# Kernel tuning notes

Hardware: AMD Instinct MI355X
Metric: run time of the kernel (lower is better)

Reference implementation:

```python
import jax, jax.numpy as jnp
import numpy as np

E, D, H, F = 3, 512, 8, 2048
B, V, L = 32, 21, 128
DH = D // H
EPS = 1e-5


def setup_inputs() -> dict:
    key = jax.random.key(0)
    ks = jax.random.split(key, 8)
    s = 0.02
    def p(k, shape):
        return (jax.random.normal(k, shape, jnp.float32) * s)
    return {
        "x": jax.random.normal(ks[0], (B, V, L, D), jnp.float32),
        "Wq": p(ks[1], (E, D, D)), "bq": jnp.zeros((E, D), jnp.float32),
        "Wk": p(ks[2], (E, D, D)), "bk": jnp.zeros((E, D), jnp.float32),
        "Wv": p(ks[3], (E, D, D)), "bv": jnp.zeros((E, D), jnp.float32),
        "Wo": p(ks[4], (E, D, D)), "bo": jnp.zeros((E, D), jnp.float32),
        "W1": p(ks[5], (E, D, F)), "b1": jnp.zeros((E, F), jnp.float32),
        "W2": p(ks[6], (E, F, D)), "b2": jnp.zeros((E, D), jnp.float32),
        "g1": jnp.ones((E, D), jnp.float32), "be1": jnp.zeros((E, D), jnp.float32),
        "g2": jnp.ones((E, D), jnp.float32), "be2": jnp.zeros((E, D), jnp.float32),
    }


def _batchnorm(x, gamma, beta):
    # x: [N, L, D]; BatchNorm1d(d_model) on x.transpose(-2,-1) == per-D-channel
    # stats over (N, L) axes (train-mode, biased variance).
    mean = jnp.mean(x, axis=(0, 1))
    var = jnp.var(x, axis=(0, 1))
    return (x - mean) * jax.lax.rsqrt(var + EPS) * gamma + beta


def _layer(x, prev_scores, Wq, bq, Wk, bk, Wv, bv, Wo, bo,
           W1, b1, W2, b2, g1, be1, g2, be2):
    N = x.shape[0]
    # multi-head projections -> [N, H, L, DH]
    q = (x @ Wq + bq).reshape(N, L, H, DH).transpose(0, 2, 1, 3)
    k = (x @ Wk + bk).reshape(N, L, H, DH).transpose(0, 2, 1, 3)
    v = (x @ Wv + bv).reshape(N, L, H, DH).transpose(0, 2, 1, 3)
    scores = jnp.einsum('nhld,nhmd->nhlm', q, k) / jnp.sqrt(jnp.float32(DH))
    if prev_scores is not None:
        scores = scores + prev_scores  # RealFormer-style residual score add
    attn = jax.nn.softmax(scores, axis=-1)
    ctx = jnp.einsum('nhlm,nhmd->nhld', attn, v)
    ctx = ctx.transpose(0, 2, 1, 3).reshape(N, L, D)
    x_ = ctx @ Wo + bo
    x = _batchnorm(x + x_, g1, be1)
    ffn = jax.nn.gelu(x @ W1 + b1, approximate=False) @ W2 + b2
    x = _batchnorm(x + ffn, g2, be2)
    return x, scores


def reference(x, Wq, bq, Wk, bk, Wv, bv, Wo, bo, W1, b1, W2, b2,
              g1, be1, g2, be2):
    h = x.reshape(-1, L, D)  # (B*V, L, D)
    scores = None
    for i in range(E):
        h, scores = _layer(h, scores,
                           Wq[i], bq[i], Wk[i], bk[i], Wv[i], bv[i],
                           Wo[i], bo[i], W1[i], b1[i], W2[i], b2[i],
                           g1[i], be1[i], g2[i], be2[i])
    return h
```

## Files before the change

### kernel.cpp

```cpp
#include <hip/hip_runtime.h>
#include <hip/hip_bf16.h>


typedef unsigned short u16;
typedef unsigned int u32;
typedef __attribute__((ext_vector_type(8))) short short8;
typedef __attribute__((ext_vector_type(4))) float floatx4;

#define DEV static __device__ __forceinline__

DEV u16 f2bf(float f) {
    union { float f; u32 u; } a; a.f = f;
    u32 r = a.u + 0x7FFF + ((a.u >> 16) & 1);
    return (u16)(r >> 16);
}
DEV float bf2f(u16 b) {
    union { u32 u; float f; } a; a.u = ((u32)b) << 16; return a.f;
}

DEV void gload16(const void* g, void* l) {
    __builtin_amdgcn_global_load_lds((const __attribute__((address_space(1))) void*)g,
                                     (__attribute__((address_space(3))) void*)l, 16, 0, 0);
}

__global__ void wtrans(const float* __restrict__ W, u16* __restrict__ out, int K, int N) {
    __shared__ float tile[32][33];
    const int k0 = blockIdx.x * 32, n0 = blockIdx.y * 32;
    const int tx = threadIdx.x & 31, ty = threadIdx.x >> 5;
#pragma unroll
    for (int j = 0; j < 4; ++j) {
        int r = ty + j * 8;
        tile[r][tx] = W[(size_t)(k0 + r) * N + n0 + tx];
    }
    __syncthreads();
#pragma unroll
    for (int j = 0; j < 4; ++j) {
        int r = ty + j * 8;
        out[(size_t)(n0 + r) * K + k0 + tx] = f2bf(tile[tx][r]);
    }
}

__global__ void bias_concat(const float* __restrict__ bq, const float* __restrict__ bk,
                            const float* __restrict__ bv, float* __restrict__ bqkv) {
    int t = blockIdx.x * 256 + threadIdx.x;
    if (t >= 3 * 1536) return;
    int e = t / 1536, c = t % 1536;
    float v = (c < 512) ? bq[e * 512 + c] : (c < 1024) ? bk[e * 512 + c - 512] : bv[e * 512 + c - 1024];
    bqkv[t] = v;
}

__global__ void xconvert(const float* __restrict__ x, u16* __restrict__ hb) {
    size_t i = ((size_t)blockIdx.x * 256 + threadIdx.x) * 8;
    float4 v0 = *(const float4*)&x[i];
    float4 v1 = *(const float4*)&x[i + 4];
    short8 o;
    o[0] = (short)f2bf(v0.x); o[1] = (short)f2bf(v0.y); o[2] = (short)f2bf(v0.z); o[3] = (short)f2bf(v0.w);
    o[4] = (short)f2bf(v1.x); o[5] = (short)f2bf(v1.y); o[6] = (short)f2bf(v1.z); o[7] = (short)f2bf(v1.w);
    *(short8*)&hb[i] = o;
}

template <int EPI>
__global__ __launch_bounds__(512)
void gemm_bt(const u16* __restrict__ A, int lda, const u16* __restrict__ Bt,
             const float* __restrict__ bias, const u16* __restrict__ res,
             u16* __restrict__ out, int N, int K) {
    __shared__ u16 sA[128 * 32];
    __shared__ u16 sB[128 * 32];
    const int tid = threadIdx.x;
    const int wave = tid >> 6, lane = tid & 63;
    const int wm = wave >> 2, wn = wave & 3;
    const int m0 = blockIdx.y * 128, n0 = blockIdx.x * 128;
    const int fr = lane & 15, fq = lane >> 4;
    const int srow = lane >> 2, scol = (lane & 3) * 8;

    floatx4 acc[4][2] = {};

    for (int k0 = 0; k0 < K; k0 += 32) {
        __syncthreads();
        {
            int ra = wave * 16 + srow;
            gload16(A + (size_t)(m0 + ra) * lda + k0 + scol, &sA[wave * 512]);
            gload16(Bt + (size_t)(n0 + ra) * K + k0 + scol, &sB[wave * 512]);
        }
        __syncthreads();
        short8 af[4], bfr[2];
#pragma unroll
        for (int m = 0; m < 4; ++m)
            af[m] = *(const short8*)&sA[(wm * 64 + m * 16 + fr) * 32 + fq * 8];
#pragma unroll
        for (int nn = 0; nn < 2; ++nn)
            bfr[nn] = *(const short8*)&sB[(wn * 32 + nn * 16 + fr) * 32 + fq * 8];
#pragma unroll
        for (int m = 0; m < 4; ++m)
#pragma unroll
            for (int nn = 0; nn < 2; ++nn)
                acc[m][nn] = __builtin_amdgcn_mfma_f32_16x16x32_bf16(af[m], bfr[nn], acc[m][nn], 0, 0, 0);
    }

#pragma unroll
    for (int nn = 0; nn < 2; ++nn) {
        int col = n0 + wn * 32 + nn * 16 + fr;
        float bv = bias[col];
#pragma unroll
        for (int m = 0; m < 4; ++m) {
            int rowb = m0 + wm * 64 + m * 16 + fq * 4;
#pragma unroll
            for (int r = 0; r < 4; ++r) {
                size_t idx = (size_t)(rowb + r) * N + col;
                float v = acc[m][nn][r] + bv;
                if (EPI == 2) {
                    v += bf2f(res[idx]);
                } else if (EPI == 1) {
                    v = 0.5f * v * (1.f + erff(v * 0.70710678118f));
                }
                out[idx] = f2bf(v);
            }
        }
    }
}

template <int HAS_PREV, int STORE_S>
__global__ __launch_bounds__(256)
void attn_kernel(u16* __restrict__ qkv, u16* __restrict__ scores) {
    const int bid = blockIdx.x;
    const int n = bid >> 3, h = bid & 7;
    const int tid = threadIdx.x, wave = tid >> 6, lane = tid & 63;
    const int wm = wave >> 1, wn = wave & 1;
    const int fr = lane & 15, fq = lane >> 4;

    __shared__ __align__(16) u16 uni[128 * 136];
    __shared__ __align__(16) u16 sV[64 * 136];
    __shared__ float sRed[128 * 2];

    u16 (*sQK)[128 * 32] = (u16(*)[128 * 32])uni;

    {
        const int t_ = wave;
        const int qk = t_ >> 1, kh = t_ & 1;
        const u16* base = qkv + (size_t)n * 128 * 1536 + qk * 512 + h * 64 + kh * 32 + (lane & 3) * 8;
        u16* dst = &sQK[t_][0];
        const int rr = lane >> 2;
#pragma unroll
        for (int c = 0; c < 8; ++c)
            gload16(base + (size_t)(c * 16 + rr) * 1536, dst + c * 512);
    }
    for (int i = 0; i < 32; ++i) {
        int idx = i * 256 + tid;
        int dh = idx & 63, m = idx >> 6;
        sV[dh * 136 + m] = qkv[(size_t)(n * 128 + m) * 1536 + 1024 + h * 64 + dh];
    }
    __syncthreads();

    floatx4 acc[4][4] = {};
#pragma unroll
    for (int kh = 0; kh < 2; ++kh) {
        short8 a[4], b[4];
#pragma unroll
        for (int m = 0; m < 4; ++m)
            a[m] = *(const short8*)&sQK[kh][(wm * 64 + m * 16 + fr) * 32 + fq * 8];
#pragma unroll
        for (int nn = 0; nn < 4; ++nn)
            b[nn] = *(const short8*)&sQK[2 + kh][(wn * 64 + nn * 16 + fr) * 32 + fq * 8];
#pragma unroll
        for (int m = 0; m < 4; ++m)
#pragma unroll
            for (int nn = 0; nn < 4; ++nn)
                acc[m][nn] = __builtin_amdgcn_mfma_f32_16x16x32_bf16(a[m], b[nn], acc[m][nn], 0, 0, 0);
    }

    const size_t sbase = (size_t)bid * 128 * 128;
#pragma unroll
    for (int m = 0; m < 4; ++m)
#pragma unroll
        for (int r = 0; r < 4; ++r) {
            int row = wm * 64 + m * 16 + fq * 4 + r;
#pragma unroll
            for (int nn = 0; nn < 4; ++nn) {
                int col = wn * 64 + nn * 16 + fr;
                float v = acc[m][nn][r] * 0.125f;
                if (HAS_PREV) v += bf2f(scores[sbase + (size_t)row * 128 + col]);
                if (STORE_S) scores[sbase + (size_t)row * 128 + col] = f2bf(v);
                acc[m][nn][r] = v;
            }
        }

#pragma unroll
    for (int m = 0; m < 4; ++m)
#pragma unroll
        for (int r = 0; r < 4; ++r) {
            float mx = fmaxf(fmaxf(acc[m][0][r], acc[m][1][r]), fmaxf(acc[m][2][r], acc[m][3][r]));
#pragma unroll
            for (int d = 1; d < 16; d <<= 1) mx = fmaxf(mx, __shfl_xor(mx, d));
            if (fr == 0) sRed[(wm * 64 + m * 16 + fq * 4 + r) * 2 + wn] = mx;
        }
    __syncthreads();

    float rmax[4][4];
#pragma unroll
    for (int m = 0; m < 4; ++m)
#pragma unroll
        for (int r = 0; r < 4; ++r) {
            int row = wm * 64 + m * 16 + fq * 4 + r;
            rmax[m][r] = fmaxf(sRed[row * 2], sRed[row * 2 + 1]);
        }
    __syncthreads();

    u16* sP = uni;
#pragma unroll
    for (int m = 0; m < 4; ++m)
#pragma unroll
        for (int r = 0; r < 4; ++r) {
            int row = wm * 64 + m * 16 + fq * 4 + r;
            float sm = 0.f;
#pragma unroll
            for (int nn = 0; nn < 4; ++nn) {
                float p = __expf(acc[m][nn][r] - rmax[m][r]);
                acc[m][nn][r] = p;
                sm += p;
            }
#pragma unroll
            for (int d = 1; d < 16; d <<= 1) sm += __shfl_xor(sm, d);
            if (fr == 0) sRed[row * 2 + wn] = sm;
#pragma unroll
            for (int nn = 0; nn < 4; ++nn)
                sP[row * 136 + wn * 64 + nn * 16 + fr] = f2bf(acc[m][nn][r]);
        }
    __syncthreads();

    floatx4 acc2[4][2] = {};
#pragma unroll
    for (int k0 = 0; k0 < 128; k0 += 32) {
        short8 a[4], b[2];
#pragma unroll
        for (int m = 0; m < 4; ++m)
            a[m] = *(const short8*)&sP[(wm * 64 + m * 16 + fr) * 136 + k0 + fq * 8];
#pragma unroll
        for (int n2 = 0; n2 < 2; ++n2)
            b[n2] = *(const short8*)&sV[(wn * 32 + n2 * 16 + fr) * 136 + k0 + fq * 8];
#pragma unroll
        for (int m = 0; m < 4; ++m)
#pragma unroll
            for (int n2 = 0; n2 < 2; ++n2)
                acc2[m][n2] = __builtin_amdgcn_mfma_f32_16x16x32_bf16(a[m], b[n2], acc2[m][n2], 0, 0, 0);
    }

#pragma unroll
    for (int m = 0; m < 4; ++m)
#pragma unroll
        for (int r = 0; r < 4; ++r) {
            int row = wm * 64 + m * 16 + fq * 4 + r;
            float inv = 1.f / (sRed[row * 2] + sRed[row * 2 + 1]);
#pragma unroll
            for (int n2 = 0; n2 < 2; ++n2) {
                int col = wn * 32 + n2 * 16 + fr;
                qkv[(size_t)(n * 128 + row) * 1536 + h * 64 + col] = f2bf(acc2[m][n2][r] * inv);
            }
        }
}

__global__ void zero_stats(float* s) { s[threadIdx.x] = 0.f; }

__global__ void bn_stats(const u16* __restrict__ y, float* __restrict__ stats, int M) {
    const int t = threadIdx.x;
    const int c0 = t * 2;
    float s0 = 0, s1 = 0, q0 = 0, q1 = 0;
    for (int r = blockIdx.x; r < M; r += gridDim.x) {
        u32 v = *(const u32*)&y[(size_t)r * 512 + c0];
        float a = bf2f((u16)(v & 0xffff)), b = bf2f((u16)(v >> 16));
        s0 += a; s1 += b; q0 += a * a; q1 += b * b;
    }
    atomicAdd(&stats[c0], s0);
    atomicAdd(&stats[c0 + 1], s1);
    atomicAdd(&stats[512 + c0], q0);
    atomicAdd(&stats[512 + c0 + 1], q1);
}

__global__ void bn_finalize(float* stats, int M) {
    int c = blockIdx.x * 256 + threadIdx.x;
    if (c >= 512) return;
    float mean = stats[c] / M;
    float var = stats[512 + c] / M - mean * mean;
    stats[c] = mean;
    stats[512 + c] = rsqrtf(var + 1e-5f);
}

template <int FINAL>
__global__ void bn_apply(const u16* __restrict__ y, const float* __restrict__ stats,
                         const float* __restrict__ gamma, const float* __restrict__ beta,
                         u16* __restrict__ outb, float* __restrict__ outf) {
    size_t i = ((size_t)blockIdx.x * 256 + threadIdx.x) * 8;
    short8 v = *(const short8*)&y[i];
    int c = (int)(i & 511);
    float o[8];
#pragma unroll
    for (int j = 0; j < 8; ++j) {
        float f = bf2f((u16)v[j]);
        o[j] = (f - stats[c + j]) * stats[512 + c + j] * gamma[c + j] + beta[c + j];
    }
    if (FINAL) {
        float4 a = { o[0], o[1], o[2], o[3] }, b = { o[4], o[5], o[6], o[7] };
        *(float4*)&outf[i] = a;
        *(float4*)&outf[i + 4] = b;
    } else {
        short8 ob;
#pragma unroll
        for (int j = 0; j < 8; ++j) ob[j] = (short)f2bf(o[j]);
        *(short8*)&outb[i] = ob;
    }
}

extern "C" void kernel_launch(void* const* d_in, const int* in_sizes, int n_in,
                              void* d_out, int out_size, void* d_ws, size_t ws_size,
                              hipStream_t stream) {
    const float* x  = (const float*)d_in[0];
    const float* Wq = (const float*)d_in[1];  const float* bq = (const float*)d_in[2];
    const float* Wk = (const float*)d_in[3];  const float* bk = (const float*)d_in[4];
    const float* Wv = (const float*)d_in[5];  const float* bv = (const float*)d_in[6];
    const float* Wo = (const float*)d_in[7];  const float* bo = (const float*)d_in[8];
    const float* W1 = (const float*)d_in[9];  const float* b1 = (const float*)d_in[10];
    const float* W2 = (const float*)d_in[11]; const float* b2 = (const float*)d_in[12];
    const float* g1 = (const float*)d_in[13]; const float* be1 = (const float*)d_in[14];
    const float* g2 = (const float*)d_in[15]; const float* be2 = (const float*)d_in[16];

    const int M = 86016;
    const int MC = 43008;

    char* ws = (char*)d_ws;
    size_t off = 0;
    auto alloc = [&](size_t bytes) -> void* {
        void* p = ws + off;
        off = (off + bytes + 255) & ~(size_t)255;
        return p;
    };
    u16* scores = (u16*)alloc((size_t)5376 * 16384 * 2);
    u16* hb     = (u16*)alloc((size_t)M * 512 * 2);
    u16* qkv    = (u16*)alloc((size_t)M * 1536 * 2);
    u16* Wqkvt  = (u16*)alloc((size_t)3 * 1536 * 512 * 2);
    u16* Wot    = (u16*)alloc((size_t)3 * 512 * 512 * 2);
    u16* W1t    = (u16*)alloc((size_t)3 * 2048 * 512 * 2);
    u16* W2t    = (u16*)alloc((size_t)3 * 512 * 2048 * 2);
    float* bqkv = (float*)alloc((size_t)3 * 1536 * 4);
    float* stats = (float*)alloc(1024 * 4);

    if (off > ws_size) return;

    for (int e = 0; e < 3; ++e) {
        wtrans<<<dim3(16, 16), 256, 0, stream>>>(Wq + (size_t)e * 512 * 512, Wqkvt + (size_t)e * 1536 * 512, 512, 512);
        wtrans<<<dim3(16, 16), 256, 0, stream>>>(Wk + (size_t)e * 512 * 512, Wqkvt + (size_t)e * 1536 * 512 + 512 * 512, 512, 512);
        wtrans<<<dim3(16, 16), 256, 0, stream>>>(Wv + (size_t)e * 512 * 512, Wqkvt + (size_t)e * 1536 * 512 + 1024 * 512, 512, 512);
        wtrans<<<dim3(16, 16), 256, 0, stream>>>(Wo + (size_t)e * 512 * 512, Wot + (size_t)e * 512 * 512, 512, 512);
        wtrans<<<dim3(16, 64), 256, 0, stream>>>(W1 + (size_t)e * 512 * 2048, W1t + (size_t)e * 2048 * 512, 512, 2048);
        wtrans<<<dim3(64, 16), 256, 0, stream>>>(W2 + (size_t)e * 2048 * 512, W2t + (size_t)e * 512 * 2048, 2048, 512);
    }
    bias_concat<<<18, 256, 0, stream>>>(bq, bk, bv, bqkv);
    xconvert<<<21504, 256, 0, stream>>>(x, hb);

    for (int e = 0; e < 3; ++e) {
        gemm_bt<0><<<dim3(12, 672), 512, 0, stream>>>(hb, 512, Wqkvt + (size_t)e * 1536 * 512,
                                                      bqkv + e * 1536, nullptr, qkv, 1536, 512);
        if (e == 0)      attn_kernel<0, 1><<<5376, 256, 0, stream>>>(qkv, scores);
        else if (e == 1) attn_kernel<1, 1><<<5376, 256, 0, stream>>>(qkv, scores);
        else             attn_kernel<1, 0><<<5376, 256, 0, stream>>>(qkv, scores);
        gemm_bt<2><<<dim3(4, 672), 512, 0, stream>>>(qkv, 1536, Wot + (size_t)e * 512 * 512,
                                                     bo + e * 512, hb, hb, 512, 512);
        zero_stats<<<1, 1024, 0, stream>>>(stats);
        bn_stats<<<512, 256, 0, stream>>>(hb, stats, M);
        bn_finalize<<<2, 256, 0, stream>>>(stats, M);
        bn_apply<0><<<21504, 256, 0, stream>>>(hb, stats, g1 + e * 512, be1 + e * 512, hb, nullptr);
        for (int c = 0; c < 2; ++c) {
            const u16* hc = hb + (size_t)c * MC * 512;
            gemm_bt<1><<<dim3(16, 336), 512, 0, stream>>>(hc, 512, W1t + (size_t)e * 2048 * 512,
                                                          b1 + e * 2048, nullptr, qkv, 2048, 512);
            gemm_bt<2><<<dim3(4, 336), 512, 0, stream>>>(qkv, 2048, W2t + (size_t)e * 512 * 2048,
                                                         b2 + e * 512, hc, (u16*)hc, 512, 2048);
        }
        zero_stats<<<1, 1024, 0, stream>>>(stats);
        bn_stats<<<512, 256, 0, stream>>>(hb, stats, M);
        bn_finalize<<<2, 256, 0, stream>>>(stats, M);
        if (e < 2)
            bn_apply<0><<<21504, 256, 0, stream>>>(hb, stats, g2 + e * 512, be2 + e * 512, hb, nullptr);
        else
            bn_apply<1><<<21504, 256, 0, stream>>>(hb, stats, g2 + e * 512, be2 + e * 512, nullptr, (float*)d_out);
    }
    (void)in_sizes; (void)n_in; (void)out_size;
}
```

Before: 3.983 ms.

## Fuse BatchNorm statistics into GEMM epilogue and vectorize attention score/V loads

BatchNorm sum and sum-of-squares are now accumulated in the residual GEMM epilogue, reduced across lanes by shuffles and added with atomics, so the separate bn_stats pass over the activations is gone. The attention kernel now loads V with 16-byte vector reads before transposing into shared memory. It also stores the residual scores in a per-thread fragment-ordered layout so they can be read and written as contiguous short8 vectors. The trade-offs are more global atomics from every GEMM tile and statistics computed from unrounded float values rather than the stored bf16.

```diff
diff --git a/kernel.cpp b/kernel.cpp
--- a/kernel.cpp
+++ b/kernel.cpp
@@ -63,7 +63,7 @@
 __global__ __launch_bounds__(512)
 void gemm_bt(const u16* __restrict__ A, int lda, const u16* __restrict__ Bt,
              const float* __restrict__ bias, const u16* __restrict__ res,
-             u16* __restrict__ out, int N, int K) {
+             u16* __restrict__ out, int N, int K, float* __restrict__ stats) {
     __shared__ u16 sA[128 * 32];
     __shared__ u16 sB[128 * 32];
     const int tid = threadIdx.x;
@@ -97,6 +97,7 @@
                 acc[m][nn] = __builtin_amdgcn_mfma_f32_16x16x32_bf16(af[m], bfr[nn], acc[m][nn], 0, 0, 0);
     }
 
+    float ssum[2] = { 0.f, 0.f }, sqsum[2] = { 0.f, 0.f };
 #pragma unroll
     for (int nn = 0; nn < 2; ++nn) {
         int col = n0 + wn * 32 + nn * 16 + fr;
@@ -110,10 +111,25 @@
                 float v = acc[m][nn][r] + bv;
                 if (EPI == 2) {
                     v += bf2f(res[idx]);
+                    ssum[nn] += v;
+                    sqsum[nn] += v * v;
                 } else if (EPI == 1) {
                     v = 0.5f * v * (1.f + erff(v * 0.70710678118f));
                 }
                 out[idx] = f2bf(v);
+            }
+        }
+    }
+    if (EPI == 2) {
+#pragma unroll
+        for (int nn = 0; nn < 2; ++nn) {
+            float s = ssum[nn], q = sqsum[nn];
+            s += __shfl_xor(s, 16); s += __shfl_xor(s, 32);
+            q += __shfl_xor(q, 16); q += __shfl_xor(q, 32);
+            if (fq == 0) {
+                int col = n0 + wn * 32 + nn * 16 + fr;
+                atomicAdd(&stats[col], s);
+                atomicAdd(&stats[512 + col], q);
             }
         }
     }
@@ -144,10 +160,17 @@
         for (int c = 0; c < 8; ++c)
             gload16(base + (size_t)(c * 16 + rr) * 1536, dst + c * 512);
     }
-    for (int i = 0; i < 32; ++i) {
-        int idx = i * 256 + tid;
-        int dh = idx & 63, m = idx >> 6;
-        sV[dh * 136 + m] = qkv[(size_t)(n * 128 + m) * 1536 + 1024 + h * 64 + dh];
+    {
+        const int mrow = tid >> 1;
+        const int dh0 = (tid & 1) * 32;
+        const u16* vsrc = qkv + (size_t)(n * 128 + mrow) * 1536 + 1024 + h * 64 + dh0;
+#pragma unroll
+        for (int j = 0; j < 4; ++j) {
+            short8 vv = *(const short8*)&vsrc[j * 8];
+#pragma unroll
+            for (int e2 = 0; e2 < 8; ++e2)
+                sV[(dh0 + j * 8 + e2) * 136 + mrow] = (u16)vv[e2];
+        }
     }
     __syncthreads();
 
@@ -168,21 +191,37 @@
                 acc[m][nn] = __builtin_amdgcn_mfma_f32_16x16x32_bf16(a[m], b[nn], acc[m][nn], 0, 0, 0);
     }
 
-    const size_t sbase = (size_t)bid * 128 * 128;
-#pragma unroll
-    for (int m = 0; m < 4; ++m)
-#pragma unroll
-        for (int r = 0; r < 4; ++r) {
-            int row = wm * 64 + m * 16 + fq * 4 + r;
-#pragma unroll
-            for (int nn = 0; nn < 4; ++nn) {
-                int col = wn * 64 + nn * 16 + fr;
+    const size_t tbase = ((size_t)bid * 256 + tid) * 64;
+#pragma unroll
+    for (int m = 0; m < 4; ++m) {
+        short8 lo, hi;
+        if (HAS_PREV) {
+            lo = *(const short8*)&scores[tbase + m * 16];
+            hi = *(const short8*)&scores[tbase + m * 16 + 8];
+        }
+#pragma unroll
+        for (int nn = 0; nn < 4; ++nn)
+#pragma unroll
+            for (int r = 0; r < 4; ++r) {
+                const int e = nn * 4 + r;
                 float v = acc[m][nn][r] * 0.125f;
-                if (HAS_PREV) v += bf2f(scores[sbase + (size_t)row * 128 + col]);
-                if (STORE_S) scores[sbase + (size_t)row * 128 + col] = f2bf(v);
+                if (HAS_PREV) v += bf2f((u16)(e < 8 ? lo[e] : hi[e - 8]));
                 acc[m][nn][r] = v;
             }
-        }
+        if (STORE_S) {
+            short8 slo, shi;
+#pragma unroll
+            for (int nn = 0; nn < 4; ++nn)
+#pragma unroll
+                for (int r = 0; r < 4; ++r) {
+                    const int e = nn * 4 + r;
+                    u16 bv = f2bf(acc[m][nn][r]);
+                    if (e < 8) slo[e] = (short)bv; else shi[e - 8] = (short)bv;
+                }
+            *(short8*)&scores[tbase + m * 16] = slo;
+            *(short8*)&scores[tbase + m * 16 + 8] = shi;
+        }
+    }
 
 #pragma unroll
     for (int m = 0; m < 4; ++m)
@@ -259,21 +298,6 @@
 }
 
 __global__ void zero_stats(float* s) { s[threadIdx.x] = 0.f; }
-
-__global__ void bn_stats(const u16* __restrict__ y, float* __restrict__ stats, int M) {
-    const int t = threadIdx.x;
-    const int c0 = t * 2;
-    float s0 = 0, s1 = 0, q0 = 0, q1 = 0;
-    for (int r = blockIdx.x; r < M; r += gridDim.x) {
-        u32 v = *(const u32*)&y[(size_t)r * 512 + c0];
-        float a = bf2f((u16)(v & 0xffff)), b = bf2f((u16)(v >> 16));
-        s0 += a; s1 += b; q0 += a * a; q1 += b * b;
-    }
-    atomicAdd(&stats[c0], s0);
-    atomicAdd(&stats[c0 + 1], s1);
-    atomicAdd(&stats[512 + c0], q0);
-    atomicAdd(&stats[512 + c0 + 1], q1);
-}
 
 __global__ void bn_finalize(float* stats, int M) {
     int c = blockIdx.x * 256 + threadIdx.x;
@@ -357,25 +381,23 @@
 
     for (int e = 0; e < 3; ++e) {
         gemm_bt<0><<<dim3(12, 672), 512, 0, stream>>>(hb, 512, Wqkvt + (size_t)e * 1536 * 512,
-                                                      bqkv + e * 1536, nullptr, qkv, 1536, 512);
+                                                      bqkv + e * 1536, nullptr, qkv, 1536, 512, nullptr);
         if (e == 0)      attn_kernel<0, 1><<<5376, 256, 0, stream>>>(qkv, scores);
         else if (e == 1) attn_kernel<1, 1><<<5376, 256, 0, stream>>>(qkv, scores);
         else             attn_kernel<1, 0><<<5376, 256, 0, stream>>>(qkv, scores);
+        zero_stats<<<1, 1024, 0, stream>>>(stats);
         gemm_bt<2><<<dim3(4, 672), 512, 0, stream>>>(qkv, 1536, Wot + (size_t)e * 512 * 512,
-                                                     bo + e * 512, hb, hb, 512, 512);
-        zero_stats<<<1, 1024, 0, stream>>>(stats);
-        bn_stats<<<512, 256, 0, stream>>>(hb, stats, M);
+                                                     bo + e * 512, hb, hb, 512, 512, stats);
         bn_finalize<<<2, 256, 0, stream>>>(stats, M);
         bn_apply<0><<<21504, 256, 0, stream>>>(hb, stats, g1 + e * 512, be1 + e * 512, hb, nullptr);
+        zero_stats<<<1, 1024, 0, stream>>>(stats);
         for (int c = 0; c < 2; ++c) {
             const u16* hc = hb + (size_t)c * MC * 512;
             gemm_bt<1><<<dim3(16, 336), 512, 0, stream>>>(hc, 512, W1t + (size_t)e * 2048 * 512,
-                                                          b1 + e * 2048, nullptr, qkv, 2048, 512);
+                                                          b1 + e * 2048, nullptr, qkv, 2048, 512, nullptr);
             gemm_bt<2><<<dim3(4, 336), 512, 0, stream>>>(qkv, 2048, W2t + (size_t)e * 512 * 2048,
-                                                         b2 + e * 512, hc, (u16*)hc, 512, 2048);
-        }
-        zero_stats<<<1, 1024, 0, stream>>>(stats);
-        bn_stats<<<512, 256, 0, stream>>>(hb, stats, M);
+                                                         b2 + e * 512, hc, (u16*)hc, 512, 2048, stats);
+        }
         bn_finalize<<<2, 256, 0, stream>>>(stats, M);
         if (e < 2)
             bn_apply<0><<<21504, 256, 0, stream>>>(hb, stats, g2 + e * 512, be2 + e * 512, hb, nullptr);
```

Measured after the change: 3.552 ms. 1.12x faster.
